# Kernel optimization log

Hardware: AMD Instinct MI355X
Metric: run time of the kernel (lower is better)

## Reference

```python
import jax, jax.numpy as jnp
import numpy as np

T, B, INPUT_DIM, HIDDEN_DIM = 256, 128, 512, 512
N_QUBITS = HIDDEN_DIM  # must match hidden_dim for the gate elementwise math


def _qlayer(v, theta):
    # Closed-form of the PennyLane circuit: RX(x_i)RX(theta_i) per wire, CNOT
    # ladder, <Z_k>.  <Z_k> = prod_{j<=k} cos(v_j + theta_j).
    return jnp.cumprod(jnp.cos(v + theta), axis=-1)


def setup_inputs() -> dict:
    key = jax.random.key(0)
    ks = jax.random.split(key, 13)
    comb = INPUT_DIM + HIDDEN_DIM
    s = 1.0 / np.sqrt(comb)
    inp = {"inputs": jax.random.normal(ks[0], (T, B, INPUT_DIM), dtype=jnp.float32)}
    names = ["forget", "input", "update", "output"]
    for n, i in zip(names, range(4)):
        inp[f"W_{n}"] = jax.random.uniform(ks[1 + 3 * i], (HIDDEN_DIM, comb), jnp.float32, -s, s)
        inp[f"b_{n}"] = jax.random.uniform(ks[2 + 3 * i], (HIDDEN_DIM,), jnp.float32, -s, s)
        inp[f"theta_{n}"] = jax.random.normal(ks[3 + 3 * i], (N_QUBITS,), dtype=jnp.float32)
    return inp


def reference(inputs, W_forget, b_forget, theta_forget,
              W_input, b_input, theta_input,
              W_update, b_update, theta_update,
              W_output, b_output, theta_output):
    Bsz = inputs.shape[1]
    h0 = jnp.zeros((Bsz, HIDDEN_DIM), dtype=inputs.dtype)
    c0 = jnp.zeros((Bsz, HIDDEN_DIM), dtype=inputs.dtype)

    def step(carry, x):
        hx, cx = carry
        comb = jnp.concatenate([x, hx], axis=1)  # [B, input+hidden]
        f = jax.nn.sigmoid(_qlayer(comb @ W_forget.T + b_forget, theta_forget))
        i = jax.nn.sigmoid(_qlayer(comb @ W_input.T + b_input, theta_input))
        g = jnp.tanh(_qlayer(comb @ W_update.T + b_update, theta_update))
        o = jax.nn.sigmoid(_qlayer(comb @ W_output.T + b_output, theta_output))
        cx = f * cx + i * g
        hx = o * jnp.tanh(cx)
        return (hx, cx), hx

    (hx, cx), outputs = jax.lax.scan(step, (h0, c0), inputs)
    return outputs, (hx, cx)
```

## Files before the change

### kernel.cpp

```cpp
#include <hip/hip_runtime.h>
#include <hip/hip_bf16.h>

#define T_STEPS 256
#define BATCH   128
#define DIN     512
#define DH      512
#define NGATE   2048
#define NCL     8
#define WPC     32
#define ROWS_CL 16
#define NWG     (NCL * WPC)

typedef __attribute__((ext_vector_type(8))) short short8;
typedef __attribute__((ext_vector_type(4))) float f32x4;
typedef unsigned long long u64;

#define OUT_HX ((size_t)T_STEPS * BATCH * DH)
#define OUT_CX (OUT_HX + (size_t)BATCH * DH)

#define WB_OFF    0
#define XB_OFF    (4 * 1024 * 1024)
#define BT_OFF    (XB_OFF + 32 * 1024 * 1024)
#define CL_OFF    (BT_OFF + 8192)
#define CL_STRIDE (160 * 1024)
#define CLV_OFF   0
#define CLH_OFF   131072
#define CLF_OFF   147456
#define CLFB_OFF  (CLF_OFF + 4096)
#define SLOT_STRIDE 32
#define BOOT_OFF  (CL_OFF + NCL * CL_STRIDE)

#define LDS_W_BYTES 131072
#define LDS_TOTAL   (LDS_W_BYTES + 4 * DH * 4)

__device__ inline ushort f2bf(float x) {
  uint u = __float_as_uint(x);
  u += 0x7fffu + ((u >> 16) & 1u);
  return (ushort)(u >> 16);
}
__device__ inline float sigm(float x) { return 1.f / (1.f + __expf(-x)); }
__device__ inline float tanhf_(float x) { return 1.f - 2.f / (1.f + __expf(2.f * x)); }

__device__ inline u64 ald64(const u64* p) {
  return __hip_atomic_load(p, __ATOMIC_RELAXED, __HIP_MEMORY_SCOPE_AGENT);
}
__device__ inline void ast32(uint* p, uint v) {
  __hip_atomic_store(p, v, __ATOMIC_RELAXED, __HIP_MEMORY_SCOPE_AGENT);
}
__device__ inline int aldi(const int* p) {
  return __hip_atomic_load(p, __ATOMIC_RELAXED, __HIP_MEMORY_SCOPE_AGENT);
}
__device__ inline void asti(int* p, int v) {
  __hip_atomic_store(p, v, __ATOMIC_RELAXED, __HIP_MEMORY_SCOPE_AGENT);
}
__device__ inline void l1inv() {
  asm volatile("buffer_inv" ::: "memory");
  asm volatile("s_waitcnt vmcnt(0)" ::: "memory");
}
template<bool L> __device__ inline void fstore(int* p, int v) {
  if constexpr (L) *(volatile int*)p = v;
  else             asti(p, v);
}
template<bool L> __device__ inline int fload(const int* p) {
  if constexpr (L) return *(volatile const int*)p;
  else             return aldi(p);
}

union U16 { u64 q[2]; short8 s; };
union UF2 { u64 q; float f[2]; };

__global__ void k_prep_w(const float* __restrict__ Wf, const float* __restrict__ Wi,
                         const float* __restrict__ Wu, const float* __restrict__ Wo,
                         ushort* __restrict__ Wb) {
  size_t i4 = ((size_t)blockIdx.x * 256 + threadIdx.x) * 4;
  if (i4 >= (size_t)NGATE * 1024) return;
  int row = (int)(i4 >> 10);
  int col = (int)(i4 & 1023);
  const float* W = (row < 512) ? Wf : (row < 1024) ? Wi : (row < 1536) ? Wu : Wo;
  int r = row & 511;
  float4 w = *(const float4*)&W[(size_t)r * 1024 + col];
  ushort4 o = make_ushort4(f2bf(w.x), f2bf(w.y), f2bf(w.z), f2bf(w.w));
  *(ushort4*)&Wb[i4] = o;
}

__global__ void k_prep_x(const float* __restrict__ X, ushort* __restrict__ Xb) {
  size_t i4 = ((size_t)blockIdx.x * 256 + threadIdx.x) * 4;
  if (i4 >= (size_t)T_STEPS * BATCH * DIN) return;
  float4 xv = *(const float4*)&X[i4];
  ushort4 o = make_ushort4(f2bf(xv.x), f2bf(xv.y), f2bf(xv.z), f2bf(xv.w));
  *(ushort4*)&Xb[i4] = o;
}

__global__ void k_prep_misc(const float* __restrict__ bf_, const float* __restrict__ tf_,
                            const float* __restrict__ bi_, const float* __restrict__ ti_,
                            const float* __restrict__ bu_, const float* __restrict__ tu_,
                            const float* __restrict__ bo_, const float* __restrict__ to_,
                            float* __restrict__ bt, char* __restrict__ clbase,
                            int* __restrict__ boot) {
  int idx = blockIdx.x * 256 + threadIdx.x;
  if (idx < NGATE) {
    int g = idx >> 9, k = idx & 511;
    const float* b = (g == 0) ? bf_ : (g == 1) ? bi_ : (g == 2) ? bu_ : bo_;
    const float* t = (g == 0) ? tf_ : (g == 1) ? ti_ : (g == 2) ? tu_ : to_;
    bt[idx] = b[k] + t[k];
  }
  if (idx < NCL * 4096) {
    int c = idx >> 12, w = idx & 4095;
    ((uint*)(clbase + (size_t)c * CL_STRIDE + CLH_OFF))[w] = 0u;
  }
  if (idx < NCL * 2048) {
    int c = idx >> 11, w = idx & 2047;
    ((int*)(clbase + (size_t)c * CL_STRIDE + CLF_OFF))[w] = 0;
  }
  if (idx < 16) boot[idx] = 0;
}

template<bool L>
__device__ __forceinline__ void run_main(
    const ushort* __restrict__ Xb, const ushort* __restrict__ Wb,
    const float* __restrict__ bt, char* cl, float* __restrict__ out,
    int cluster, int mem, ushort* wlds, float* lds_g) {
  const int tid  = threadIdx.x;
  const int lane = tid & 63;
  const int wave = tid >> 6;

  float*  v_cl  = (float*)(cl + CLV_OFF);
  u64*    h_cl  = (u64*)(cl + CLH_OFF);
  uint*   h_cl32= (uint*)(cl + CLH_OFF);
  int*    slotA = (int*)(cl + CLF_OFF);
  int*    slotB = (int*)(cl + CLFB_OFF);

  const int nb    = mem * 64 + wave * 16;
  const int ar    = lane & 15;
  const int kx    = (lane >> 4) << 3;
  const int crow0 = cluster * ROWS_CL;
  const int row   = crow0 + mem;
  const int wrow  = wave * 16 + ar;

  {
    const char* wsrc = (const char*)(Wb + (size_t)(mem * 64) * 1024);
#pragma unroll
    for (int it = 0; it < 32; ++it) {
      int idx16 = it * 256 + tid;
      int r  = idx16 >> 7;
      int kb = (idx16 & 127) << 4;
      short8 w = *(const short8*)(wsrc + (size_t)r * 2048 + kb);
      *(short8*)((char*)wlds + (size_t)r * 2048 + (kb ^ ((r & 7) << 4))) = w;
    }
  }
#define WFRAG(KT) (*(const short8*)((const char*)wlds + (size_t)wrow * 2048 + \
                    ((((KT) * 64) + (kx << 1)) ^ ((ar & 7) << 4))))

  float btr[8];
  {
    const int e0 = lane << 3;
#pragma unroll
    for (int j = 0; j < 8; ++j) btr[j] = bt[wave * DH + e0 + j];
  }
  __syncthreads();

  float c0 = 0.f, c1 = 0.f;
  f32x4 accE = {0.f, 0.f, 0.f, 0.f}, accO = {0.f, 0.f, 0.f, 0.f};

#define XPART(TT) do {                                                        \
    accE = (f32x4){0.f, 0.f, 0.f, 0.f};                                       \
    accO = (f32x4){0.f, 0.f, 0.f, 0.f};                                       \
    const ushort* Ax = Xb + ((size_t)(TT) * BATCH + crow0 + ar) * DIN + kx;   \
    _Pragma("unroll")                                                         \
    for (int kt = 0; kt < 16; kt += 2) {                                      \
      short8 a0 = *(const short8*)(Ax + kt * 32);                             \
      short8 a1 = *(const short8*)(Ax + (kt + 1) * 32);                       \
      accE = __builtin_amdgcn_mfma_f32_16x16x32_bf16(a0, WFRAG(kt), accE, 0, 0, 0);     \
      accO = __builtin_amdgcn_mfma_f32_16x16x32_bf16(a1, WFRAG(kt + 1), accO, 0, 0, 0); \
    }                                                                         \
  } while (0)

  XPART(0);

  for (int t = 0; t < T_STEPS; ++t) {
    const int ep = t + 1;
    {
      U16 af[16];
#pragma unroll
      for (int kt = 0; kt < 16; ++kt) {
        const u64* p = h_cl + (((size_t)ar * DH + kt * 32 + kx) >> 2);
        if constexpr (L) { af[kt].q[0] = p[0];       af[kt].q[1] = p[1]; }
        else             { af[kt].q[0] = ald64(p);   af[kt].q[1] = ald64(p + 1); }
      }
#pragma unroll
      for (int kt = 0; kt < 16; kt += 2) {
        accE = __builtin_amdgcn_mfma_f32_16x16x32_bf16(af[kt].s,     WFRAG(16 + kt),     accE, 0, 0, 0);
        accO = __builtin_amdgcn_mfma_f32_16x16x32_bf16(af[kt + 1].s, WFRAG(16 + kt + 1), accO, 0, 0, 0);
      }
    }
    {
      const int rbase = (lane >> 4) << 2;
      float* vp = v_cl + (size_t)rbase * NGATE + nb + ar;
#pragma unroll
      for (int r = 0; r < 4; ++r) {
        float val = accE[r] + accO[r];
        if constexpr (L) vp[(size_t)r * NGATE] = val;
        else             ast32((uint*)&vp[(size_t)r * NGATE], __float_as_uint(val));
      }
    }
    __syncthreads();
    if (tid == 0) fstore<L>(&slotA[mem * SLOT_STRIDE], ep);

    if (mem < ROWS_CL) {
      if (wave == 0) {
        for (;;) {
          if constexpr (L) l1inv();
          int s = (lane < WPC) ? fload<L>(&slotA[lane * SLOT_STRIDE]) : ep;
          if (__all(s >= ep)) break;
          __builtin_amdgcn_s_sleep(1);
        }
        if constexpr (L) l1inv();
      }
      __syncthreads();
      asm volatile("" ::: "memory");
      {
        const int g  = wave;
        const int e0 = lane << 3;
        const u64* vr = (const u64*)(v_cl + (size_t)mem * NGATE + g * DH + e0);
        UF2 w0, w1, w2, w3;
        if constexpr (L) { w0.q = vr[0]; w1.q = vr[1]; w2.q = vr[2]; w3.q = vr[3]; }
        else { w0.q = ald64(vr); w1.q = ald64(vr + 1); w2.q = ald64(vr + 2); w3.q = ald64(vr + 3); }
        float p0 = __cosf(w0.f[0] + btr[0]);
        float p1 = __cosf(w0.f[1] + btr[1]);
        float p2 = __cosf(w1.f[0] + btr[2]);
        float p3 = __cosf(w1.f[1] + btr[3]);
        float p4 = __cosf(w2.f[0] + btr[4]);
        float p5 = __cosf(w2.f[1] + btr[5]);
        float p6 = __cosf(w3.f[0] + btr[6]);
        float p7 = __cosf(w3.f[1] + btr[7]);
        float q0 = p0, q1 = q0 * p1, q2 = q1 * p2, q3 = q2 * p3;
        float q4 = q3 * p4, q5 = q4 * p5, q6 = q5 * p6, q7 = q6 * p7;
        float a = q7;
#pragma unroll
        for (int off = 1; off < 64; off <<= 1) {
          float o = __shfl_up(a, off);
          a = (lane >= off) ? a * o : a;
        }
        float ex = __shfl_up(a, 1);
        ex = (lane == 0) ? 1.f : ex;
        float G0 = ex * q0, G1 = ex * q1, G2 = ex * q2, G3 = ex * q3;
        float G4 = ex * q4, G5 = ex * q5, G6 = ex * q6, G7 = ex * q7;
        float4 r0, r1;
        if (g == 2) {
          r0 = make_float4(tanhf_(G0), tanhf_(G1), tanhf_(G2), tanhf_(G3));
          r1 = make_float4(tanhf_(G4), tanhf_(G5), tanhf_(G6), tanhf_(G7));
        } else {
          r0 = make_float4(sigm(G0), sigm(G1), sigm(G2), sigm(G3));
          r1 = make_float4(sigm(G4), sigm(G5), sigm(G6), sigm(G7));
        }
        *(float4*)&lds_g[g * DH + e0]     = r0;
        *(float4*)&lds_g[g * DH + e0 + 4] = r1;
      }
      __syncthreads();
      {
        const int k = tid << 1;
        float f0 = lds_g[0 * DH + k], f1 = lds_g[0 * DH + k + 1];
        float i0 = lds_g[1 * DH + k], i1 = lds_g[1 * DH + k + 1];
        float u0 = lds_g[2 * DH + k], u1 = lds_g[2 * DH + k + 1];
        float o0 = lds_g[3 * DH + k], o1 = lds_g[3 * DH + k + 1];
        c0 = f0 * c0 + i0 * u0;
        c1 = f1 * c1 + i1 * u1;
        float h0 = o0 * tanhf_(c0);
        float h1 = o1 * tanhf_(c1);
        uint hbits = ((uint)f2bf(h1) << 16) | (uint)f2bf(h0);
        if constexpr (L) h_cl32[mem * 256 + tid] = hbits;
        else             ast32(&h_cl32[mem * 256 + tid], hbits);
        __syncthreads();
        if (tid == 0) fstore<L>(&slotB[mem * SLOT_STRIDE], ep);
        float2 hp = make_float2(h0, h1);
        *(float2*)&out[((size_t)t * BATCH + row) * DH + k] = hp;
        if (t == T_STEPS - 1) {
          *(float2*)&out[OUT_HX + (size_t)row * DH + k] = hp;
          float2 cp = make_float2(c0, c1);
          *(float2*)&out[OUT_CX + (size_t)row * DH + k] = cp;
        }
      }
      __syncthreads();
    }

    if (t + 1 < T_STEPS) {
      XPART(t + 1);
      if (wave == 0) {
        for (;;) {
          if constexpr (L) l1inv();
          int s = (lane < ROWS_CL) ? fload<L>(&slotB[lane * SLOT_STRIDE]) : ep;
          if (__all(s >= ep)) break;
          __builtin_amdgcn_s_sleep(1);
        }
        if constexpr (L) l1inv();
      }
      __syncthreads();
      asm volatile("" ::: "memory");
    }
  }
#undef XPART
#undef WFRAG
}

__global__ __launch_bounds__(256, 1) void qlstm_main(
    const ushort* __restrict__ Xb, const ushort* __restrict__ Wb,
    const float* __restrict__ bt, char* __restrict__ clbase,
    int* __restrict__ boot, float* __restrict__ out) {
  extern __shared__ char smem[];
  ushort* wlds  = (ushort*)smem;
  float*  lds_g = (float*)(smem + LDS_W_BYTES);

  __shared__ int shboot[4];
  const int tid = threadIdx.x;

  if (tid == 0) {
    uint xcc;
    asm volatile("s_getreg_b32 %0, hwreg(HW_REG_XCC_ID)" : "=s"(xcc));
    xcc &= 7;
    int slot = __hip_atomic_fetch_add(&boot[xcc], 1, __ATOMIC_RELAXED, __HIP_MEMORY_SCOPE_AGENT);
    __hip_atomic_fetch_add(&boot[8], 1, __ATOMIC_RELAXED, __HIP_MEMORY_SCOPE_AGENT);
    while (__hip_atomic_load(&boot[8], __ATOMIC_RELAXED, __HIP_MEMORY_SCOPE_AGENT) < NWG)
      __builtin_amdgcn_s_sleep(8);
    int ok = 1;
#pragma unroll
    for (int c2 = 0; c2 < NCL; ++c2)
      ok &= (__hip_atomic_load(&boot[c2], __ATOMIC_RELAXED, __HIP_MEMORY_SCOPE_AGENT) == WPC);
    shboot[0] = (int)xcc;
    shboot[1] = slot;
    shboot[2] = ok;
  }
  __syncthreads();
  const int local_ok = shboot[2];
  const int cluster  = local_ok ? shboot[0] : ((int)blockIdx.x & 7);
  const int mem      = local_ok ? shboot[1] : ((int)blockIdx.x >> 3);
  char* cl = clbase + (size_t)cluster * CL_STRIDE;

  if (local_ok)
    run_main<true>(Xb, Wb, bt, cl, out, cluster, mem, wlds, lds_g);
  else
    run_main<false>(Xb, Wb, bt, cl, out, cluster, mem, wlds, lds_g);
}

extern "C" void kernel_launch(void* const* d_in, const int* in_sizes, int n_in,
                              void* d_out, int out_size, void* d_ws, size_t ws_size,
                              hipStream_t stream) {
  const float* X  = (const float*)d_in[0];
  const float* Wf = (const float*)d_in[1];
  const float* bf = (const float*)d_in[2];
  const float* tf = (const float*)d_in[3];
  const float* Wi = (const float*)d_in[4];
  const float* bi = (const float*)d_in[5];
  const float* ti = (const float*)d_in[6];
  const float* Wu = (const float*)d_in[7];
  const float* bu = (const float*)d_in[8];
  const float* tu = (const float*)d_in[9];
  const float* Wo = (const float*)d_in[10];
  const float* bo = (const float*)d_in[11];
  const float* to = (const float*)d_in[12];

  char* ws = (char*)d_ws;
  ushort* Wb     = (ushort*)(ws + WB_OFF);
  ushort* Xb     = (ushort*)(ws + XB_OFF);
  float*  bt     = (float*)(ws + BT_OFF);
  char*   clbase = ws + CL_OFF;
  int*    boot   = (int*)(ws + BOOT_OFF);
  float*  out    = (float*)d_out;

  static bool attr_set = false;
  if (!attr_set) {
    hipFuncSetAttribute((const void*)qlstm_main,
                        hipFuncAttributeMaxDynamicSharedMemorySize, LDS_TOTAL);
    attr_set = true;
  }

  k_prep_w<<<dim3((NGATE * 1024 / 4 + 255) / 256), dim3(256), 0, stream>>>(Wf, Wi, Wu, Wo, Wb);
  k_prep_x<<<dim3((T_STEPS * BATCH * DIN / 4 + 255) / 256), dim3(256), 0, stream>>>(X, Xb);
  k_prep_misc<<<dim3(256), dim3(256), 0, stream>>>(bf, tf, bi, ti, bu, tu, bo, to, bt, clbase, boot);
  qlstm_main<<<dim3(NWG), dim3(256), LDS_TOTAL, stream>>>(Xb, Wb, bt, clbase, boot, out);
}
```

Measured before the change: 1.635 ms.

## Replicate gate epilogue in every workgroup to drop second cluster barrier

Each of the 32 workgroups in a cluster now computes the cumprod/activation epilogue for all 16 batch rows redundantly and keeps h in its own LDS. This removes the second barrier per timestep (slotB) and the global h exchange through the cluster buffer. The cost is 16x redundant transcendental and scan work per workgroup, more registers for the per-row cell state, and full reads of the cluster's gate buffer by every workgroup. The x-projection for the next step is moved before the barrier wait so it overlaps the wait.

```diff
diff --git a/kernel.cpp b/kernel.cpp
--- a/kernel.cpp
+++ b/kernel.cpp
@@ -13,6 +13,7 @@
 
 typedef __attribute__((ext_vector_type(8))) short short8;
 typedef __attribute__((ext_vector_type(4))) float f32x4;
+typedef __attribute__((ext_vector_type(4))) uint  u32x4;
 typedef unsigned long long u64;
 
 #define OUT_HX ((size_t)T_STEPS * BATCH * DH)
@@ -24,14 +25,13 @@
 #define CL_OFF    (BT_OFF + 8192)
 #define CL_STRIDE (160 * 1024)
 #define CLV_OFF   0
-#define CLH_OFF   131072
-#define CLF_OFF   147456
-#define CLFB_OFF  (CLF_OFF + 4096)
+#define CLF_OFF   131072
 #define SLOT_STRIDE 32
 #define BOOT_OFF  (CL_OFF + NCL * CL_STRIDE)
 
 #define LDS_W_BYTES 131072
-#define LDS_TOTAL   (LDS_W_BYTES + 4 * DH * 4)
+#define LDS_H_BYTES 16384
+#define LDS_TOTAL   (LDS_W_BYTES + LDS_H_BYTES)
 
 __device__ inline ushort f2bf(float x) {
   uint u = __float_as_uint(x);
@@ -66,7 +66,6 @@
   else             return aldi(p);
 }
 
-union U16 { u64 q[2]; short8 s; };
 union UF2 { u64 q; float f[2]; };
 
 __global__ void k_prep_w(const float* __restrict__ Wf, const float* __restrict__ Wi,
@@ -104,12 +103,8 @@
     const float* t = (g == 0) ? tf_ : (g == 1) ? ti_ : (g == 2) ? tu_ : to_;
     bt[idx] = b[k] + t[k];
   }
-  if (idx < NCL * 4096) {
-    int c = idx >> 12, w = idx & 4095;
-    ((uint*)(clbase + (size_t)c * CL_STRIDE + CLH_OFF))[w] = 0u;
-  }
-  if (idx < NCL * 2048) {
-    int c = idx >> 11, w = idx & 2047;
+  if (idx < NCL * 1024) {
+    int c = idx >> 10, w = idx & 1023;
     ((int*)(clbase + (size_t)c * CL_STRIDE + CLF_OFF))[w] = 0;
   }
   if (idx < 16) boot[idx] = 0;
@@ -119,22 +114,21 @@
 __device__ __forceinline__ void run_main(
     const ushort* __restrict__ Xb, const ushort* __restrict__ Wb,
     const float* __restrict__ bt, char* cl, float* __restrict__ out,
-    int cluster, int mem, ushort* wlds, float* lds_g) {
+    int cluster, int mem, char* smem) {
+  ushort* wlds = (ushort*)smem;
+  char*   hlds = smem + LDS_W_BYTES;
+
   const int tid  = threadIdx.x;
   const int lane = tid & 63;
   const int wave = tid >> 6;
 
-  float*  v_cl  = (float*)(cl + CLV_OFF);
-  u64*    h_cl  = (u64*)(cl + CLH_OFF);
-  uint*   h_cl32= (uint*)(cl + CLH_OFF);
-  int*    slotA = (int*)(cl + CLF_OFF);
-  int*    slotB = (int*)(cl + CLFB_OFF);
+  float* v_cl  = (float*)(cl + CLV_OFF);
+  int*   slotA = (int*)(cl + CLF_OFF);
 
   const int nb    = mem * 64 + wave * 16;
   const int ar    = lane & 15;
   const int kx    = (lane >> 4) << 3;
   const int crow0 = cluster * ROWS_CL;
-  const int row   = crow0 + mem;
   const int wrow  = wave * 16 + ar;
 
   {
@@ -150,16 +144,24 @@
   }
 #define WFRAG(KT) (*(const short8*)((const char*)wlds + (size_t)wrow * 2048 + \
                     ((((KT) * 64) + (kx << 1)) ^ ((ar & 7) << 4))))
-
-  float btr[8];
-  {
-    const int e0 = lane << 3;
-#pragma unroll
-    for (int j = 0; j < 8; ++j) btr[j] = bt[wave * DH + e0 + j];
-  }
+#define HFRAG(KT) (*(const short8*)(hlds + ar * 1024 + \
+                    ((((KT) * 64) + (kx << 1)) ^ ((ar & 7) << 4))))
+
+  for (int i = tid; i < LDS_H_BYTES / 4; i += 256) ((uint*)hlds)[i] = 0u;
+
+  float btr[4][8];
+#pragma unroll
+  for (int g = 0; g < 4; ++g)
+#pragma unroll
+    for (int j = 0; j < 8; ++j) btr[g][j] = bt[g * DH + lane * 8 + j];
   __syncthreads();
 
-  float c0 = 0.f, c1 = 0.f;
+  float cst[4][8];
+#pragma unroll
+  for (int ri = 0; ri < 4; ++ri)
+#pragma unroll
+    for (int j = 0; j < 8; ++j) cst[ri][j] = 0.f;
+
   f32x4 accE = {0.f, 0.f, 0.f, 0.f}, accO = {0.f, 0.f, 0.f, 0.f};
 
 #define XPART(TT) do {                                                        \
@@ -179,19 +181,12 @@
 
   for (int t = 0; t < T_STEPS; ++t) {
     const int ep = t + 1;
-    {
-      U16 af[16];
-#pragma unroll
-      for (int kt = 0; kt < 16; ++kt) {
-        const u64* p = h_cl + (((size_t)ar * DH + kt * 32 + kx) >> 2);
-        if constexpr (L) { af[kt].q[0] = p[0];       af[kt].q[1] = p[1]; }
-        else             { af[kt].q[0] = ald64(p);   af[kt].q[1] = ald64(p + 1); }
-      }
-#pragma unroll
-      for (int kt = 0; kt < 16; kt += 2) {
-        accE = __builtin_amdgcn_mfma_f32_16x16x32_bf16(af[kt].s,     WFRAG(16 + kt),     accE, 0, 0, 0);
-        accO = __builtin_amdgcn_mfma_f32_16x16x32_bf16(af[kt + 1].s, WFRAG(16 + kt + 1), accO, 0, 0, 0);
-      }
+#pragma unroll
+    for (int kt = 0; kt < 16; kt += 2) {
+      short8 a0 = HFRAG(kt);
+      short8 a1 = HFRAG(kt + 1);
+      accE = __builtin_amdgcn_mfma_f32_16x16x32_bf16(a0, WFRAG(16 + kt),     accE, 0, 0, 0);
+      accO = __builtin_amdgcn_mfma_f32_16x16x32_bf16(a1, WFRAG(16 + kt + 1), accO, 0, 0, 0);
     }
     {
       const int rbase = (lane >> 4) << 2;
@@ -206,36 +201,52 @@
     __syncthreads();
     if (tid == 0) fstore<L>(&slotA[mem * SLOT_STRIDE], ep);
 
-    if (mem < ROWS_CL) {
-      if (wave == 0) {
-        for (;;) {
-          if constexpr (L) l1inv();
-          int s = (lane < WPC) ? fload<L>(&slotA[lane * SLOT_STRIDE]) : ep;
-          if (__all(s >= ep)) break;
-          __builtin_amdgcn_s_sleep(1);
+    if (t + 1 < T_STEPS) XPART(t + 1);
+
+    if (wave == 0) {
+      for (;;) {
+        if constexpr (L) l1inv();
+        int s = (lane < WPC) ? fload<L>(&slotA[lane * SLOT_STRIDE]) : ep;
+        if (__all(s >= ep)) break;
+        __builtin_amdgcn_s_sleep(1);
+      }
+      if constexpr (L) l1inv();
+    }
+    __syncthreads();
+    asm volatile("" ::: "memory");
+
+#pragma unroll
+    for (int ri = 0; ri < 4; ++ri) {
+      const int r = wave * 4 + ri;
+      float vv[4][8];
+      {
+        const float* vr = v_cl + (size_t)r * NGATE + lane * 8;
+#pragma unroll
+        for (int g = 0; g < 4; ++g) {
+          if constexpr (L) {
+            f32x4 w0 = *(const f32x4*)(vr + g * DH);
+            f32x4 w1 = *(const f32x4*)(vr + g * DH + 4);
+            vv[g][0] = w0[0]; vv[g][1] = w0[1]; vv[g][2] = w0[2]; vv[g][3] = w0[3];
+            vv[g][4] = w1[0]; vv[g][5] = w1[1]; vv[g][6] = w1[2]; vv[g][7] = w1[3];
+          } else {
+            const u64* vq = (const u64*)(vr + g * DH);
+            UF2 wa, wb, wc, wd;
+            wa.q = ald64(vq);     wb.q = ald64(vq + 1);
+            wc.q = ald64(vq + 2); wd.q = ald64(vq + 3);
+            vv[g][0] = wa.f[0]; vv[g][1] = wa.f[1]; vv[g][2] = wb.f[0]; vv[g][3] = wb.f[1];
+            vv[g][4] = wc.f[0]; vv[g][5] = wc.f[1]; vv[g][6] = wd.f[0]; vv[g][7] = wd.f[1];
+          }
         }
-        if constexpr (L) l1inv();
-      }
-      __syncthreads();
-      asm volatile("" ::: "memory");
-      {
-        const int g  = wave;
-        const int e0 = lane << 3;
-        const u64* vr = (const u64*)(v_cl + (size_t)mem * NGATE + g * DH + e0);
-        UF2 w0, w1, w2, w3;
-        if constexpr (L) { w0.q = vr[0]; w1.q = vr[1]; w2.q = vr[2]; w3.q = vr[3]; }
-        else { w0.q = ald64(vr); w1.q = ald64(vr + 1); w2.q = ald64(vr + 2); w3.q = ald64(vr + 3); }
-        float p0 = __cosf(w0.f[0] + btr[0]);
-        float p1 = __cosf(w0.f[1] + btr[1]);
-        float p2 = __cosf(w1.f[0] + btr[2]);
-        float p3 = __cosf(w1.f[1] + btr[3]);
-        float p4 = __cosf(w2.f[0] + btr[4]);
-        float p5 = __cosf(w2.f[1] + btr[5]);
-        float p6 = __cosf(w3.f[0] + btr[6]);
-        float p7 = __cosf(w3.f[1] + btr[7]);
-        float q0 = p0, q1 = q0 * p1, q2 = q1 * p2, q3 = q2 * p3;
-        float q4 = q3 * p4, q5 = q4 * p5, q6 = q5 * p6, q7 = q6 * p7;
-        float a = q7;
+      }
+      float f8[8], i8[8], u8[8], o8[8];
+#pragma unroll
+      for (int g = 0; g < 4; ++g) {
+        float q[8];
+        q[0] = __cosf(vv[g][0] + btr[g][0]);
+#pragma unroll
+        for (int j = 1; j < 8; ++j)
+          q[j] = q[j - 1] * __cosf(vv[g][j] + btr[g][j]);
+        float a = q[7];
 #pragma unroll
         for (int off = 1; off < 64; off <<= 1) {
           float o = __shfl_up(a, off);
@@ -243,63 +254,53 @@
         }
         float ex = __shfl_up(a, 1);
         ex = (lane == 0) ? 1.f : ex;
-        float G0 = ex * q0, G1 = ex * q1, G2 = ex * q2, G3 = ex * q3;
-        float G4 = ex * q4, G5 = ex * q5, G6 = ex * q6, G7 = ex * q7;
-        float4 r0, r1;
-        if (g == 2) {
-          r0 = make_float4(tanhf_(G0), tanhf_(G1), tanhf_(G2), tanhf_(G3));
-          r1 = make_float4(tanhf_(G4), tanhf_(G5), tanhf_(G6), tanhf_(G7));
-        } else {
-          r0 = make_float4(sigm(G0), sigm(G1), sigm(G2), sigm(G3));
-          r1 = make_float4(sigm(G4), sigm(G5), sigm(G6), sigm(G7));
+#pragma unroll
+        for (int j = 0; j < 8; ++j) {
+          float G = ex * q[j];
+          float act = (g == 2) ? tanhf_(G) : sigm(G);
+          if (g == 0) f8[j] = act;
+          else if (g == 1) i8[j] = act;
+          else if (g == 2) u8[j] = act;
+          else o8[j] = act;
         }
-        *(float4*)&lds_g[g * DH + e0]     = r0;
-        *(float4*)&lds_g[g * DH + e0 + 4] = r1;
-      }
-      __syncthreads();
+      }
+      float h8[8];
+#pragma unroll
+      for (int j = 0; j < 8; ++j) {
+        float cc = f8[j] * cst[ri][j] + i8[j] * u8[j];
+        cst[ri][j] = cc;
+        h8[j] = o8[j] * tanhf_(cc);
+      }
       {
-        const int k = tid << 1;
-        float f0 = lds_g[0 * DH + k], f1 = lds_g[0 * DH + k + 1];
-        float i0 = lds_g[1 * DH + k], i1 = lds_g[1 * DH + k + 1];
-        float u0 = lds_g[2 * DH + k], u1 = lds_g[2 * DH + k + 1];
-        float o0 = lds_g[3 * DH + k], o1 = lds_g[3 * DH + k + 1];
-        c0 = f0 * c0 + i0 * u0;
-        c1 = f1 * c1 + i1 * u1;
-        float h0 = o0 * tanhf_(c0);
-        float h1 = o1 * tanhf_(c1);
-        uint hbits = ((uint)f2bf(h1) << 16) | (uint)f2bf(h0);
-        if constexpr (L) h_cl32[mem * 256 + tid] = hbits;
-        else             ast32(&h_cl32[mem * 256 + tid], hbits);
-        __syncthreads();
-        if (tid == 0) fstore<L>(&slotB[mem * SLOT_STRIDE], ep);
-        float2 hp = make_float2(h0, h1);
-        *(float2*)&out[((size_t)t * BATCH + row) * DH + k] = hp;
+        u32x4 hp;
+#pragma unroll
+        for (int j2 = 0; j2 < 4; ++j2)
+          hp[j2] = (uint)f2bf(h8[2 * j2]) | ((uint)f2bf(h8[2 * j2 + 1]) << 16);
+        *(u32x4*)(hlds + r * 1024 + ((lane * 16) ^ ((r & 7) << 4))) = hp;
+      }
+      if (mem == r) {
+        float* op = out + ((size_t)t * BATCH + crow0 + r) * DH + lane * 8;
+        f32x4 o0 = {h8[0], h8[1], h8[2], h8[3]};
+        f32x4 o1 = {h8[4], h8[5], h8[6], h8[7]};
+        *(f32x4*)op = o0;
+        *(f32x4*)(op + 4) = o1;
         if (t == T_STEPS - 1) {
-          *(float2*)&out[OUT_HX + (size_t)row * DH + k] = hp;
-          float2 cp = make_float2(c0, c1);
-          *(float2*)&out[OUT_CX + (size_t)row * DH + k] = cp;
+          float* hxp = out + OUT_HX + (size_t)(crow0 + r) * DH + lane * 8;
+          *(f32x4*)hxp = o0;
+          *(f32x4*)(hxp + 4) = o1;
+          float* cxp = out + OUT_CX + (size_t)(crow0 + r) * DH + lane * 8;
+          f32x4 c0v = {cst[ri][0], cst[ri][1], cst[ri][2], cst[ri][3]};
+          f32x4 c1v = {cst[ri][4], cst[ri][5], cst[ri][6], cst[ri][7]};
+          *(f32x4*)cxp = c0v;
+          *(f32x4*)(cxp + 4) = c1v;
         }
       }
-      __syncthreads();
-    }
-
-    if (t + 1 < T_STEPS) {
-      XPART(t + 1);
-      if (wave == 0) {
-        for (;;) {
-          if constexpr (L) l1inv();
-          int s = (lane < ROWS_CL) ? fload<L>(&slotB[lane * SLOT_STRIDE]) : ep;
-          if (__all(s >= ep)) break;
-          __builtin_amdgcn_s_sleep(1);
-        }
-        if constexpr (L) l1inv();
-      }
-      __syncthreads();
-      asm volatile("" ::: "memory");
-    }
+    }
+    __syncthreads();
   }
 #undef XPART
 #undef WFRAG
+#undef HFRAG
 }
 
 __global__ __launch_bounds__(256, 1) void qlstm_main(
@@ -307,9 +308,6 @@
     const float* __restrict__ bt, char* __restrict__ clbase,
     int* __restrict__ boot, float* __restrict__ out) {
   extern __shared__ char smem[];
-  ushort* wlds  = (ushort*)smem;
-  float*  lds_g = (float*)(smem + LDS_W_BYTES);
-
   __shared__ int shboot[4];
   const int tid = threadIdx.x;
 
@@ -336,9 +334,9 @@
   char* cl = clbase + (size_t)cluster * CL_STRIDE;
 
   if (local_ok)
-    run_main<true>(Xb, Wb, bt, cl, out, cluster, mem, wlds, lds_g);
+    run_main<true>(Xb, Wb, bt, cl, out, cluster, mem, smem);
   else
-    run_main<false>(Xb, Wb, bt, cl, out, cluster, mem, wlds, lds_g);
+    run_main<false>(Xb, Wb, bt, cl, out, cluster, mem, smem);
 }
 
 extern "C" void kernel_launch(void* const* d_in, const int* in_sizes, int n_in,
```

Measured after the change: 3.775 ms. +130.9%, slower.
